# Performance work log

Measured on AMD Instinct MI355X. Metric: run time of the kernel, lower is better.

Reference implementation:

```python
import jax, jax.numpy as jnp
import numpy as np
import math

D_MODEL = 1024
NUM_HEADS = 16
D_KEY = D_MODEL // NUM_HEADS  # 64, used only for the softmax scale
B, S = 4, 2048


def setup_inputs() -> dict:
    key = jax.random.key(0)
    ks = jax.random.split(key, 7)
    scale = 1.0 / math.sqrt(D_MODEL)
    x = jax.random.normal(ks[0], (B, S, D_MODEL), dtype=jnp.float32)
    # torch.nn.Linear params: weight [out, in], bias [out]
    Wq = jax.random.normal(ks[1], (D_MODEL, D_MODEL), dtype=jnp.float32) * scale
    bq = jax.random.normal(ks[2], (D_MODEL,), dtype=jnp.float32) * scale
    Wk = jax.random.normal(ks[3], (D_MODEL, D_MODEL), dtype=jnp.float32) * scale
    bk = jax.random.normal(ks[4], (D_MODEL,), dtype=jnp.float32) * scale
    Wv = jax.random.normal(ks[5], (D_MODEL, D_MODEL), dtype=jnp.float32) * scale
    bv = jax.random.normal(ks[6], (D_MODEL,), dtype=jnp.float32) * scale
    return {"x": x, "Wq": Wq, "bq": bq, "Wk": Wk, "bk": bk, "Wv": Wv, "bv": bv}


def reference(x, Wq, bq, Wk, bk, Wv, bv):
    # Q, K, V projections (torch Linear: x @ W.T + b)
    Q = jnp.einsum('bsd,ed->bse', x, Wq) + bq  # [B,S,D]
    K = jnp.einsum('bsd,ed->bse', x, Wk) + bk
    V = jnp.einsum('bsd,ed->bse', x, Wv) + bv
    inv_sqrt_dk = 1.0 / math.sqrt(D_KEY)
    # full-width attention (no head split, as in the source forward)
    scores = jnp.einsum('bqd,bkd->bqk', Q, K) * inv_sqrt_dk  # [B,S,S]
    weights = jax.nn.softmax(scores, axis=-1)
    return jnp.einsum('bqk,bkd->bqd', weights, V)  # [B,S,D]
```

## Files before the change

kernel.cpp:

```cpp
#include <hip/hip_runtime.h>
#include <stdint.h>

#define S_LEN 2048
#define DMODEL 1024
#define NBATCH 4
#define MROWS (NBATCH * S_LEN)

typedef __bf16 bf16x8 __attribute__((ext_vector_type(8)));
typedef float f32x4 __attribute__((ext_vector_type(4)));

__device__ __forceinline__ unsigned short f2bf(float f) {
  unsigned int x = __builtin_bit_cast(unsigned int, f);
  x += 0x7FFFu + ((x >> 16) & 1u);
  return (unsigned short)(x >> 16);
}

template <int N>
__device__ __forceinline__ void waitvm() {
  static_assert(N <= 8, "vmcnt range");
  if constexpr (N < 0) {}
  else if constexpr (N == 0) asm volatile("s_waitcnt vmcnt(0)" ::: "memory");
  else if constexpr (N == 1) asm volatile("s_waitcnt vmcnt(1)" ::: "memory");
  else if constexpr (N == 2) asm volatile("s_waitcnt vmcnt(2)" ::: "memory");
  else if constexpr (N == 3) asm volatile("s_waitcnt vmcnt(3)" ::: "memory");
  else if constexpr (N == 4) asm volatile("s_waitcnt vmcnt(4)" ::: "memory");
  else if constexpr (N == 5) asm volatile("s_waitcnt vmcnt(5)" ::: "memory");
  else if constexpr (N == 6) asm volatile("s_waitcnt vmcnt(6)" ::: "memory");
  else if constexpr (N == 7) asm volatile("s_waitcnt vmcnt(7)" ::: "memory");
  else asm volatile("s_waitcnt vmcnt(8)" ::: "memory");
}
#define BARRIER() do { __builtin_amdgcn_s_barrier(); asm volatile("" ::: "memory"); } while (0)
#define LGKM0() do { asm volatile("s_waitcnt lgkmcnt(0)" ::: "memory"); \
                     __builtin_amdgcn_sched_barrier(0); } while (0)

__global__ void cvt_kernel(const float* __restrict__ src, ushort4* __restrict__ dst, int n4) {
  int i = blockIdx.x * blockDim.x + threadIdx.x;
  if (i < n4) {
    float4 v = reinterpret_cast<const float4*>(src)[i];
    ushort4 o;
    o.x = f2bf(v.x); o.y = f2bf(v.y); o.z = f2bf(v.z); o.w = f2bf(v.w);
    dst[i] = o;
  }
}

__global__ void prep_kernel(const float* __restrict__ Wq, const float* __restrict__ Wk,
                            const float* __restrict__ Wv, const float* __restrict__ bq,
                            const float* __restrict__ bk, ushort4* __restrict__ Wqkb,
                            ushort4* __restrict__ Wvb, float4* __restrict__ bqk) {
  const int NW = DMODEL * DMODEL / 4;
  int i = blockIdx.x * blockDim.x + threadIdx.x;
  float4 v;
  if (i < NW) v = reinterpret_cast<const float4*>(Wq)[i];
  else if (i < 2 * NW) v = reinterpret_cast<const float4*>(Wk)[i - NW];
  else v = reinterpret_cast<const float4*>(Wv)[i - 2 * NW];
  ushort4 o;
  o.x = f2bf(v.x); o.y = f2bf(v.y); o.z = f2bf(v.z); o.w = f2bf(v.w);
  if (i < 2 * NW) Wqkb[i] = o;
  else Wvb[i - 2 * NW] = o;
  if (i < 512) bqk[i] = (i < 256) ? reinterpret_cast<const float4*>(bq)[i]
                                  : reinterpret_cast<const float4*>(bk)[i - 256];
}

template <int BM_, int EP, int NT>
__global__ __launch_bounds__(512, 2) void gemm8(
    const unsigned short* __restrict__ A, const unsigned short* __restrict__ Bm,
    void* __restrict__ Cp, const float* __restrict__ bias,
    int lda, int ldb, int ldc, float scale,
    long zsA, long zsB, long zsC) {
  constexpr int BN_ = 256;
  constexpr int BK = 64;
  constexpr int RA = BM_ / 128;
  constexpr int HALF_A = (BM_ / 2) * 128;
  constexpr int HALF_B = 128 * 128;
  constexpr int ATILE = BM_ * 128;
  constexpr int BTILE = BN_ * 128;
  constexpr int MREP = BM_ / 32;
  constexpr int MQ = MREP / 2;
  constexpr int VPRO = (BM_ == 256) ? 4 : 3;
  constexpr int W_PA = (BM_ == 256) ? 6 : 4;
  constexpr int W_PB = (BM_ == 256) ? 6 : 5;
  constexpr int W_PC = (BM_ == 256) ? 4 : 3;
  constexpr int VDA  = (BM_ == 256) ? 2 : 1;

  __shared__ alignas(16) char lds[(ATILE + BTILE) * 2];

  const int tid = threadIdx.x;
  const int l = tid & 63;
  const int w = tid >> 6;
  const int wm = w >> 2;
  const int wn = w & 3;

  const int gx = gridDim.x;
  const int nwg = gridDim.x * gridDim.y;
  int n = blockIdx.y * gx + blockIdx.x;
  int n2 = (n & 7) * (nwg >> 3) + (n >> 3);
  const int tileM = (n2 / gx) * BM_;
  const int tileN = (n2 % gx) * BN_;

  const int z = blockIdx.z;
  const unsigned short* Ab = A + (size_t)z * zsA;
  const unsigned short* Bb = Bm + (size_t)z * zsB;

  const int srow = l >> 3;
  const int scol = (((l & 7) ^ srow) * 16);

  auto stageA = [&](int buf, int t, int h) {
#pragma unroll
    for (int r = 0; r < RA; ++r) {
      int row = h * (BM_ / 2) + r * 64 + w * 8 + srow;
      const char* g = (const char*)(Ab + (size_t)(tileM + row) * lda + t * BK) + scol;
      char* d = lds + buf * (ATILE + BTILE) + h * HALF_A + r * 8192 + w * 1024;
      __builtin_amdgcn_global_load_lds(
          (const __attribute__((address_space(1))) void*)g,
          (__attribute__((address_space(3))) void*)d, 16, 0, 0);
    }
  };
  auto stageB = [&](int buf, int t, int h) {
#pragma unroll
    for (int r = 0; r < 2; ++r) {
      int row = h * 128 + r * 64 + w * 8 + srow;
      const char* g = (const char*)(Bb + (size_t)(tileN + row) * ldb + t * BK) + scol;
      char* d = lds + buf * (ATILE + BTILE) + ATILE + h * HALF_B + r * 8192 + w * 1024;
      __builtin_amdgcn_global_load_lds(
          (const __attribute__((address_space(1))) void*)g,
          (__attribute__((address_space(3))) void*)d, 16, 0, 0);
    }
  };

  f32x4 acc[MREP][4];
#pragma unroll
  for (int m = 0; m < MREP; ++m)
#pragma unroll
    for (int nn = 0; nn < 4; ++nn) acc[m][nn] = f32x4{0.f, 0.f, 0.f, 0.f};

  const int frow = l & 15;
  auto rdA = [&](int buf, int mh, int m, int kk) -> bf16x8 {
    int row = mh * (BM_ / 2) + wm * (BM_ / 4) + m * 16 + frow;
    int col = (kk * 64 + ((l >> 4) * 16)) ^ ((row & 7) << 4);
    return *reinterpret_cast<const bf16x8*>(lds + buf * (ATILE + BTILE) + row * 128 + col);
  };
  auto rdB = [&](int buf, int nh, int nn, int kk) -> bf16x8 {
    int row = nh * 128 + wn * 32 + nn * 16 + frow;
    int col = (kk * 64 + ((l >> 4) * 16)) ^ ((row & 7) << 4);
    return *reinterpret_cast<const bf16x8*>(lds + buf * (ATILE + BTILE) + ATILE + row * 128 + col);
  };

  bf16x8 avF[MQ][2];
  bf16x8 bv0[2][2], bv1[2][2];

  auto rdAfull = [&](int buf, int mh) {
#pragma unroll
    for (int m = 0; m < MQ; ++m)
#pragma unroll
      for (int kk = 0; kk < 2; ++kk) avF[m][kk] = rdA(buf, mh, m, kk);
  };
  auto rdBfull = [&](int buf, int nh, bf16x8 (&bv)[2][2]) {
#pragma unroll
    for (int nn = 0; nn < 2; ++nn)
#pragma unroll
      for (int kk = 0; kk < 2; ++kk) bv[nn][kk] = rdB(buf, nh, nn, kk);
  };
  auto mfc = [&](int mh, bf16x8 (&bv)[2][2], int nh) {
    __builtin_amdgcn_s_setprio(1);
#pragma unroll
    for (int kk = 0; kk < 2; ++kk)
#pragma unroll
      for (int m = 0; m < MQ; ++m)
#pragma unroll
        for (int nn = 0; nn < 2; ++nn)
          acc[mh * MQ + m][nh * 2 + nn] = __builtin_amdgcn_mfma_f32_16x16x32_bf16(
              avF[m][kk], bv[nn][kk], acc[mh * MQ + m][nh * 2 + nn], 0, 0, 0);
    __builtin_amdgcn_s_setprio(0);
  };
  auto mfc2 = [&](int mh) {
    __builtin_amdgcn_s_setprio(1);
#pragma unroll
    for (int kk = 0; kk < 2; ++kk)
#pragma unroll
      for (int m = 0; m < MQ; ++m) {
#pragma unroll
        for (int nn = 0; nn < 2; ++nn)
          acc[mh * MQ + m][2 + nn] = __builtin_amdgcn_mfma_f32_16x16x32_bf16(
              avF[m][kk], bv1[nn][kk], acc[mh * MQ + m][2 + nn], 0, 0, 0);
#pragma unroll
        for (int nn = 0; nn < 2; ++nn)
          acc[mh * MQ + m][nn] = __builtin_amdgcn_mfma_f32_16x16x32_bf16(
              avF[m][kk], bv0[nn][kk], acc[mh * MQ + m][nn], 0, 0, 0);
      }
    __builtin_amdgcn_s_setprio(0);
  };

  stageA(0, 0, 0);
  stageB(0, 0, 0);
  stageB(0, 0, 1);
  stageA(0, 0, 1);
  waitvm<VPRO>();
  BARRIER();

#pragma unroll 2
  for (int t = 0; t < NT - 1; ++t) {
    const int buf = t & 1, nb = buf ^ 1;
    rdAfull(buf, 0); rdBfull(buf, 0, bv0);
    stageA(nb, t + 1, 0); stageB(nb, t + 1, 0);
    waitvm<W_PA>(); BARRIER(); LGKM0();
    mfc(0, bv0, 0);
    rdBfull(buf, 1, bv1);
    stageB(nb, t + 1, 1);
    waitvm<W_PB>(); BARRIER(); LGKM0();
    mfc(0, bv1, 1);
    rdAfull(buf, 1);
    stageA(nb, t + 1, 1);
    waitvm<W_PC>(); BARRIER(); LGKM0();
    mfc2(1);
  }
  {
    const int buf = (NT - 1) & 1;
    rdAfull(buf, 0); rdBfull(buf, 0, bv0);
    waitvm<VDA>(); BARRIER(); LGKM0();
    mfc(0, bv0, 0);
    rdBfull(buf, 1, bv1);
    waitvm<0>(); BARRIER(); LGKM0();
    mfc(0, bv1, 1);
    rdAfull(buf, 1);
    LGKM0();
    mfc2(1);
  }

  const int lr = (l >> 4) * 4;
  const int lc = l & 15;
#pragma unroll
  for (int mh = 0; mh < 2; ++mh) {
#pragma unroll
    for (int m = 0; m < MQ; ++m) {
#pragma unroll
      for (int nh = 0; nh < 2; ++nh) {
#pragma unroll
        for (int nn = 0; nn < 2; ++nn) {
          int gr = tileM + mh * (BM_ / 2) + wm * (BM_ / 4) + m * 16 + lr;
          int gc = tileN + nh * 128 + wn * 32 + nn * 16 + lc;
          f32x4 v = acc[mh * MQ + m][nh * 2 + nn];
          if constexpr (EP == 0 || EP == 3) {
            unsigned short* C = (unsigned short*)Cp + (size_t)z * zsC;
#pragma unroll
            for (int j = 0; j < 4; ++j) {
              float bb = (EP == 0) ? bias[gc] : bias[gr + j];
              C[(size_t)(gr + j) * ldc + gc] = f2bf(v[j] + bb);
            }
          } else {
            float* C = (float*)Cp + (size_t)z * zsC;
#pragma unroll
            for (int j = 0; j < 4; ++j)
              C[(size_t)(gr + j) * ldc + gc] = (EP == 1) ? v[j] * scale : v[j];
          }
        }
      }
    }
  }
}

__global__ __launch_bounds__(256) void softmax_kernel(const float* __restrict__ Sb,
                                                      unsigned short* __restrict__ P) {
  const size_t row = blockIdx.x;
  const float* sp = Sb + row * S_LEN;
  const int t = threadIdx.x;
  const int wid = t >> 6, lane = t & 63;
  float4 v0 = reinterpret_cast<const float4*>(sp)[t * 2];
  float4 v1 = reinterpret_cast<const float4*>(sp)[t * 2 + 1];
  float s[8] = {v0.x, v0.y, v0.z, v0.w, v1.x, v1.y, v1.z, v1.w};
  float mx = s[0];
#pragma unroll
  for (int i = 1; i < 8; ++i) mx = fmaxf(mx, s[i]);
#pragma unroll
  for (int o = 32; o > 0; o >>= 1) mx = fmaxf(mx, __shfl_xor(mx, o));
  __shared__ float redm[4];
  __shared__ float reds[4];
  if (lane == 0) redm[wid] = mx;
  __syncthreads();
  mx = fmaxf(fmaxf(redm[0], redm[1]), fmaxf(redm[2], redm[3]));
  float e[8];
  float sum = 0.f;
#pragma unroll
  for (int i = 0; i < 8; ++i) { e[i] = __expf(s[i] - mx); sum += e[i]; }
#pragma unroll
  for (int o = 32; o > 0; o >>= 1) sum += __shfl_xor(sum, o);
  if (lane == 0) reds[wid] = sum;
  __syncthreads();
  sum = reds[0] + reds[1] + reds[2] + reds[3];
  float inv = 1.0f / sum;
  ushort4 o0, o1;
  o0.x = f2bf(e[0] * inv); o0.y = f2bf(e[1] * inv); o0.z = f2bf(e[2] * inv); o0.w = f2bf(e[3] * inv);
  o1.x = f2bf(e[4] * inv); o1.y = f2bf(e[5] * inv); o1.z = f2bf(e[6] * inv); o1.w = f2bf(e[7] * inv);
  ushort4* dp = reinterpret_cast<ushort4*>(P + row * S_LEN);
  dp[t * 2] = o0;
  dp[t * 2 + 1] = o1;
}

extern "C" void kernel_launch(void* const* d_in, const int* in_sizes, int n_in,
                              void* d_out, int out_size, void* d_ws, size_t ws_size,
                              hipStream_t stream) {
  (void)in_sizes; (void)n_in; (void)out_size;
  const float* x = (const float*)d_in[0];
  const float* Wq = (const float*)d_in[1];
  const float* bq = (const float*)d_in[2];
  const float* Wk = (const float*)d_in[3];
  const float* bk = (const float*)d_in[4];
  const float* Wv = (const float*)d_in[5];
  const float* bv = (const float*)d_in[6];
  float* out = (float*)d_out;

  if (ws_size < 141557760ull) return;
  char* ws = (char*)d_ws;
  unsigned short* xb   = (unsigned short*)(ws);
  unsigned short* Wqkb = (unsigned short*)(ws + 16777216);
  unsigned short* Wvb  = (unsigned short*)(ws + 20971520);
  float*          bqk  = (float*)(ws + 23068672);
  unsigned short* QKb  = (unsigned short*)(ws + 24117248);
  float*          Sb   = (float*)(ws + 57671680);
  unsigned short* Vt   = (unsigned short*)(ws + 124780544);
  unsigned short* P    = QKb;

  cvt_kernel<<<dim3(MROWS * DMODEL / 4 / 256), 256, 0, stream>>>(x, (ushort4*)xb, MROWS * DMODEL / 4);
  prep_kernel<<<dim3(3 * DMODEL * DMODEL / 4 / 256), 256, 0, stream>>>(
      Wq, Wk, Wv, bq, bk, (ushort4*)Wqkb, (ushort4*)Wvb, (float4*)bqk);

  gemm8<256, 0, 16><<<dim3(8, 32, 1), 512, 0, stream>>>(
      xb, Wqkb, QKb, bqk, 1024, 1024, 2048, 1.f, 0, 0, 0);

  gemm8<128, 3, 16><<<dim3(8, 8, 4), 512, 0, stream>>>(
      Wvb, xb, Vt, bv, 1024, 1024, 2048, 1.f,
      0, (long)S_LEN * DMODEL, (long)DMODEL * S_LEN);

  gemm8<256, 1, 16><<<dim3(8, 8, 4), 512, 0, stream>>>(
      QKb, QKb + 1024, Sb, nullptr, 2048, 2048, 2048, 0.125f,
      (long)S_LEN * 2048, (long)S_LEN * 2048, (long)S_LEN * S_LEN);

  softmax_kernel<<<dim3(MROWS), 256, 0, stream>>>(Sb, P);

  gemm8<128, 2, 32><<<dim3(4, 16, 4), 512, 0, stream>>>(
      P, Vt, out, nullptr, 2048, 2048, 1024, 1.f,
      (long)S_LEN * S_LEN, (long)DMODEL * S_LEN, (long)S_LEN * DMODEL);
}
```

Measured before the change: 165.9 us.

## Add 16-wave 256x256 GEMM kernel for QK projection and scores; merge prep kernels

Introduces gemm16, a 1024-thread (16 waves) 256x256-tile bf16 MFMA GEMM with a split-phase double-buffered LDS pipeline and XOR-swizzled direct-to-LDS loads. It replaces gemm8 for the fused Q/K projection and for the QK^T score GEMM. The two conversion kernels for x and the weights are also merged into one launch. The aim is more waves per tile to hide latency and one less launch, at the cost of one workgroup per CU, more barriers, and uncoalesced scalar epilogue stores.

```diff
diff --git a/kernel.cpp b/kernel.cpp
--- a/kernel.cpp
+++ b/kernel.cpp
@@ -33,32 +33,208 @@
 #define LGKM0() do { asm volatile("s_waitcnt lgkmcnt(0)" ::: "memory"); \
                      __builtin_amdgcn_sched_barrier(0); } while (0)
 
-__global__ void cvt_kernel(const float* __restrict__ src, ushort4* __restrict__ dst, int n4) {
-  int i = blockIdx.x * blockDim.x + threadIdx.x;
-  if (i < n4) {
-    float4 v = reinterpret_cast<const float4*>(src)[i];
-    ushort4 o;
-    o.x = f2bf(v.x); o.y = f2bf(v.y); o.z = f2bf(v.z); o.w = f2bf(v.w);
-    dst[i] = o;
-  }
-}
-
-__global__ void prep_kernel(const float* __restrict__ Wq, const float* __restrict__ Wk,
-                            const float* __restrict__ Wv, const float* __restrict__ bq,
-                            const float* __restrict__ bk, ushort4* __restrict__ Wqkb,
-                            ushort4* __restrict__ Wvb, float4* __restrict__ bqk) {
+__global__ void prep_all_kernel(const float* __restrict__ x, const float* __restrict__ Wq,
+                                const float* __restrict__ Wk, const float* __restrict__ Wv,
+                                const float* __restrict__ bq, const float* __restrict__ bk,
+                                ushort4* __restrict__ xb, ushort4* __restrict__ Wqkb,
+                                ushort4* __restrict__ Wvb, float4* __restrict__ bqk) {
+  const int NX = MROWS * DMODEL / 4;
   const int NW = DMODEL * DMODEL / 4;
   int i = blockIdx.x * blockDim.x + threadIdx.x;
   float4 v;
-  if (i < NW) v = reinterpret_cast<const float4*>(Wq)[i];
-  else if (i < 2 * NW) v = reinterpret_cast<const float4*>(Wk)[i - NW];
-  else v = reinterpret_cast<const float4*>(Wv)[i - 2 * NW];
-  ushort4 o;
-  o.x = f2bf(v.x); o.y = f2bf(v.y); o.z = f2bf(v.z); o.w = f2bf(v.w);
-  if (i < 2 * NW) Wqkb[i] = o;
-  else Wvb[i - 2 * NW] = o;
-  if (i < 512) bqk[i] = (i < 256) ? reinterpret_cast<const float4*>(bq)[i]
-                                  : reinterpret_cast<const float4*>(bk)[i - 256];
+  if (i < NX) {
+    v = reinterpret_cast<const float4*>(x)[i];
+    ushort4 o; o.x = f2bf(v.x); o.y = f2bf(v.y); o.z = f2bf(v.z); o.w = f2bf(v.w);
+    xb[i] = o;
+  } else {
+    int j = i - NX;
+    if (j < NW) v = reinterpret_cast<const float4*>(Wq)[j];
+    else if (j < 2 * NW) v = reinterpret_cast<const float4*>(Wk)[j - NW];
+    else v = reinterpret_cast<const float4*>(Wv)[j - 2 * NW];
+    ushort4 o; o.x = f2bf(v.x); o.y = f2bf(v.y); o.z = f2bf(v.z); o.w = f2bf(v.w);
+    if (j < 2 * NW) Wqkb[j] = o;
+    else Wvb[j - 2 * NW] = o;
+    if (j < 512) bqk[j] = (j < 256) ? reinterpret_cast<const float4*>(bq)[j]
+                                    : reinterpret_cast<const float4*>(bk)[j - 256];
+  }
+}
+
+template <int EP, int NT>
+__global__ __launch_bounds__(1024, 1) void gemm16(
+    const unsigned short* __restrict__ A, const unsigned short* __restrict__ Bm,
+    void* __restrict__ Cp, const float* __restrict__ bias,
+    int lda, int ldb, int ldc, float scale,
+    long zsA, long zsB, long zsC) {
+  constexpr int BK = 64;
+  constexpr int ATILE = 256 * 128;
+  constexpr int TILE2 = ATILE * 2;
+  constexpr int HALF = 128 * 128;
+
+  __shared__ alignas(16) char lds[TILE2 * 2];
+
+  const int tid = threadIdx.x;
+  const int l = tid & 63;
+  const int w = tid >> 6;
+  const int wm = w >> 2;
+  const int wn = w & 3;
+
+  const int gx = gridDim.x;
+  const int nwg = gridDim.x * gridDim.y;
+  int n = blockIdx.y * gx + blockIdx.x;
+  int n2 = (n & 7) * (nwg >> 3) + (n >> 3);
+  const int tileM = (n2 / gx) * 256;
+  const int tileN = (n2 % gx) * 256;
+
+  const int z = blockIdx.z;
+  const unsigned short* Ab = A + (size_t)z * zsA;
+  const unsigned short* Bb = Bm + (size_t)z * zsB;
+
+  const int srow = l >> 3;
+  const int scol = (((l & 7) ^ srow) * 16);
+
+  auto stageA = [&](int buf, int t, int h) {
+    int row = h * 128 + w * 8 + srow;
+    const char* g = (const char*)(Ab + (size_t)(tileM + row) * lda + t * BK) + scol;
+    char* d = lds + buf * TILE2 + h * HALF + w * 1024;
+    __builtin_amdgcn_global_load_lds(
+        (const __attribute__((address_space(1))) void*)g,
+        (__attribute__((address_space(3))) void*)d, 16, 0, 0);
+  };
+  auto stageB = [&](int buf, int t, int h) {
+    int row = h * 128 + w * 8 + srow;
+    const char* g = (const char*)(Bb + (size_t)(tileN + row) * ldb + t * BK) + scol;
+    char* d = lds + buf * TILE2 + ATILE + h * HALF + w * 1024;
+    __builtin_amdgcn_global_load_lds(
+        (const __attribute__((address_space(1))) void*)g,
+        (__attribute__((address_space(3))) void*)d, 16, 0, 0);
+  };
+
+  f32x4 acc[4][4];
+#pragma unroll
+  for (int m = 0; m < 4; ++m)
+#pragma unroll
+    for (int nn = 0; nn < 4; ++nn) acc[m][nn] = f32x4{0.f, 0.f, 0.f, 0.f};
+
+  const int frow = l & 15;
+  auto rdA = [&](int buf, int mh, int m, int kk) -> bf16x8 {
+    int row = mh * 128 + wm * 32 + m * 16 + frow;
+    int col = (kk * 64 + ((l >> 4) * 16)) ^ ((row & 7) << 4);
+    return *reinterpret_cast<const bf16x8*>(lds + buf * TILE2 + row * 128 + col);
+  };
+  auto rdB = [&](int buf, int nh, int nn, int kk) -> bf16x8 {
+    int row = nh * 128 + wn * 32 + nn * 16 + frow;
+    int col = (kk * 64 + ((l >> 4) * 16)) ^ ((row & 7) << 4);
+    return *reinterpret_cast<const bf16x8*>(lds + buf * TILE2 + ATILE + row * 128 + col);
+  };
+
+  bf16x8 avF[2][2];
+  bf16x8 bv0[2][2], bv1[2][2];
+
+  auto rdAfull = [&](int buf, int mh) {
+#pragma unroll
+    for (int m = 0; m < 2; ++m)
+#pragma unroll
+      for (int kk = 0; kk < 2; ++kk) avF[m][kk] = rdA(buf, mh, m, kk);
+  };
+  auto rdBfull = [&](int buf, int nh, bf16x8 (&bv)[2][2]) {
+#pragma unroll
+    for (int nn = 0; nn < 2; ++nn)
+#pragma unroll
+      for (int kk = 0; kk < 2; ++kk) bv[nn][kk] = rdB(buf, nh, nn, kk);
+  };
+  auto mfc = [&](int mh, bf16x8 (&bv)[2][2], int nh) {
+    __builtin_amdgcn_s_setprio(1);
+#pragma unroll
+    for (int kk = 0; kk < 2; ++kk)
+#pragma unroll
+      for (int m = 0; m < 2; ++m)
+#pragma unroll
+        for (int nn = 0; nn < 2; ++nn)
+          acc[mh * 2 + m][nh * 2 + nn] = __builtin_amdgcn_mfma_f32_16x16x32_bf16(
+              avF[m][kk], bv[nn][kk], acc[mh * 2 + m][nh * 2 + nn], 0, 0, 0);
+    __builtin_amdgcn_s_setprio(0);
+  };
+  auto mfc2 = [&](int mh) {
+    __builtin_amdgcn_s_setprio(1);
+#pragma unroll
+    for (int kk = 0; kk < 2; ++kk)
+#pragma unroll
+      for (int m = 0; m < 2; ++m) {
+#pragma unroll
+        for (int nn = 0; nn < 2; ++nn)
+          acc[mh * 2 + m][2 + nn] = __builtin_amdgcn_mfma_f32_16x16x32_bf16(
+              avF[m][kk], bv1[nn][kk], acc[mh * 2 + m][2 + nn], 0, 0, 0);
+#pragma unroll
+        for (int nn = 0; nn < 2; ++nn)
+          acc[mh * 2 + m][nn] = __builtin_amdgcn_mfma_f32_16x16x32_bf16(
+              avF[m][kk], bv0[nn][kk], acc[mh * 2 + m][nn], 0, 0, 0);
+      }
+    __builtin_amdgcn_s_setprio(0);
+  };
+
+  stageA(0, 0, 0);
+  stageB(0, 0, 0);
+  stageB(0, 0, 1);
+  stageA(0, 0, 1);
+  waitvm<2>();
+  BARRIER();
+
+#pragma unroll 2
+  for (int t = 0; t < NT - 1; ++t) {
+    const int buf = t & 1, nb = buf ^ 1;
+    rdAfull(buf, 0); rdBfull(buf, 0, bv0);
+    stageA(nb, t + 1, 0); stageB(nb, t + 1, 0);
+    waitvm<3>(); BARRIER(); LGKM0();
+    mfc(0, bv0, 0);
+    rdBfull(buf, 1, bv1);
+    stageB(nb, t + 1, 1);
+    waitvm<3>(); BARRIER(); LGKM0();
+    mfc(0, bv1, 1);
+    rdAfull(buf, 1);
+    stageA(nb, t + 1, 1);
+    waitvm<2>(); BARRIER(); LGKM0();
+    mfc2(1);
+  }
+  {
+    const int buf = (NT - 1) & 1;
+    rdAfull(buf, 0); rdBfull(buf, 0, bv0);
+    waitvm<1>(); BARRIER(); LGKM0();
+    mfc(0, bv0, 0);
+    rdBfull(buf, 1, bv1);
+    waitvm<0>(); BARRIER(); LGKM0();
+    mfc(0, bv1, 1);
+    rdAfull(buf, 1);
+    LGKM0();
+    mfc2(1);
+  }
+
+  const int lr = (l >> 4) * 4;
+  const int lc = l & 15;
+#pragma unroll
+  for (int mh = 0; mh < 2; ++mh) {
+#pragma unroll
+    for (int m = 0; m < 2; ++m) {
+#pragma unroll
+      for (int nh = 0; nh < 2; ++nh) {
+#pragma unroll
+        for (int nn = 0; nn < 2; ++nn) {
+          int gr = tileM + mh * 128 + wm * 32 + m * 16 + lr;
+          int gc = tileN + nh * 128 + wn * 32 + nn * 16 + lc;
+          f32x4 v = acc[mh * 2 + m][nh * 2 + nn];
+          if constexpr (EP == 0) {
+            unsigned short* C = (unsigned short*)Cp + (size_t)z * zsC;
+            float bb = bias[gc];
+#pragma unroll
+            for (int j = 0; j < 4; ++j) C[(size_t)(gr + j) * ldc + gc] = f2bf(v[j] + bb);
+          } else {
+            float* C = (float*)Cp + (size_t)z * zsC;
+#pragma unroll
+            for (int j = 0; j < 4; ++j) C[(size_t)(gr + j) * ldc + gc] = v[j] * scale;
+          }
+        }
+      }
+    }
+  }
 }
 
 template <int BM_, int EP, int NT>
@@ -319,18 +495,18 @@
   unsigned short* Vt   = (unsigned short*)(ws + 124780544);
   unsigned short* P    = QKb;
 
-  cvt_kernel<<<dim3(MROWS * DMODEL / 4 / 256), 256, 0, stream>>>(x, (ushort4*)xb, MROWS * DMODEL / 4);
-  prep_kernel<<<dim3(3 * DMODEL * DMODEL / 4 / 256), 256, 0, stream>>>(
-      Wq, Wk, Wv, bq, bk, (ushort4*)Wqkb, (ushort4*)Wvb, (float4*)bqk);
-
-  gemm8<256, 0, 16><<<dim3(8, 32, 1), 512, 0, stream>>>(
+  const int NX = MROWS * DMODEL / 4, NW = DMODEL * DMODEL / 4;
+  prep_all_kernel<<<dim3((NX + 3 * NW) / 256), 256, 0, stream>>>(
+      x, Wq, Wk, Wv, bq, bk, (ushort4*)xb, (ushort4*)Wqkb, (ushort4*)Wvb, (float4*)bqk);
+
+  gemm16<0, 16><<<dim3(8, 32, 1), 1024, 0, stream>>>(
       xb, Wqkb, QKb, bqk, 1024, 1024, 2048, 1.f, 0, 0, 0);
 
   gemm8<128, 3, 16><<<dim3(8, 8, 4), 512, 0, stream>>>(
       Wvb, xb, Vt, bv, 1024, 1024, 2048, 1.f,
       0, (long)S_LEN * DMODEL, (long)DMODEL * S_LEN);
 
-  gemm8<256, 1, 16><<<dim3(8, 8, 4), 512, 0, stream>>>(
+  gemm16<1, 16><<<dim3(8, 8, 4), 1024, 0, stream>>>(
       QKb, QKb + 1024, Sb, nullptr, 2048, 2048, 2048, 0.125f,
       (long)S_LEN * 2048, (long)S_LEN * 2048, (long)S_LEN * S_LEN);
 
```

Measured after the change: 171.3 us. 3.3% more time.

## Merge conversion kernels and simplify GEMM pipeline to one barrier per K-step

Applied to the files above, without the earlier changes.

Combines the x conversion and weight/bias prep kernels into a single launch, removing one kernel launch. In the bf16 GEMM main loop, the three staged vmcnt waits and barriers per K-iteration are replaced by a single full drain (lgkmcnt(0), vmcnt(0)) and one barrier at the end of each iteration. The sched_barrier fences are dropped, so the compiler is free to reorder LDS reads and MFMAs. This cuts barrier count, but a full vmcnt(0) drain per iteration reduces how much global-to-LDS prefetch overlaps with compute, and it loses the hand-tuned interleaving.

```diff
diff --git a/kernel.cpp b/kernel.cpp
--- a/kernel.cpp
+++ b/kernel.cpp
@@ -30,35 +30,32 @@
   else asm volatile("s_waitcnt vmcnt(8)" ::: "memory");
 }
 #define BARRIER() do { __builtin_amdgcn_s_barrier(); asm volatile("" ::: "memory"); } while (0)
-#define LGKM0() do { asm volatile("s_waitcnt lgkmcnt(0)" ::: "memory"); \
-                     __builtin_amdgcn_sched_barrier(0); } while (0)
-
-__global__ void cvt_kernel(const float* __restrict__ src, ushort4* __restrict__ dst, int n4) {
-  int i = blockIdx.x * blockDim.x + threadIdx.x;
-  if (i < n4) {
-    float4 v = reinterpret_cast<const float4*>(src)[i];
-    ushort4 o;
-    o.x = f2bf(v.x); o.y = f2bf(v.y); o.z = f2bf(v.z); o.w = f2bf(v.w);
-    dst[i] = o;
-  }
-}
-
-__global__ void prep_kernel(const float* __restrict__ Wq, const float* __restrict__ Wk,
-                            const float* __restrict__ Wv, const float* __restrict__ bq,
-                            const float* __restrict__ bk, ushort4* __restrict__ Wqkb,
-                            ushort4* __restrict__ Wvb, float4* __restrict__ bqk) {
+#define LGKM0() asm volatile("s_waitcnt lgkmcnt(0)" ::: "memory")
+
+__global__ void prep_all_kernel(const float* __restrict__ x, const float* __restrict__ Wq,
+                                const float* __restrict__ Wk, const float* __restrict__ Wv,
+                                const float* __restrict__ bq, const float* __restrict__ bk,
+                                ushort4* __restrict__ xb, ushort4* __restrict__ Wqkb,
+                                ushort4* __restrict__ Wvb, float4* __restrict__ bqk) {
+  const int NX = MROWS * DMODEL / 4;
   const int NW = DMODEL * DMODEL / 4;
   int i = blockIdx.x * blockDim.x + threadIdx.x;
   float4 v;
-  if (i < NW) v = reinterpret_cast<const float4*>(Wq)[i];
-  else if (i < 2 * NW) v = reinterpret_cast<const float4*>(Wk)[i - NW];
-  else v = reinterpret_cast<const float4*>(Wv)[i - 2 * NW];
-  ushort4 o;
-  o.x = f2bf(v.x); o.y = f2bf(v.y); o.z = f2bf(v.z); o.w = f2bf(v.w);
-  if (i < 2 * NW) Wqkb[i] = o;
-  else Wvb[i - 2 * NW] = o;
-  if (i < 512) bqk[i] = (i < 256) ? reinterpret_cast<const float4*>(bq)[i]
-                                  : reinterpret_cast<const float4*>(bk)[i - 256];
+  if (i < NX) {
+    v = reinterpret_cast<const float4*>(x)[i];
+    ushort4 o; o.x = f2bf(v.x); o.y = f2bf(v.y); o.z = f2bf(v.z); o.w = f2bf(v.w);
+    xb[i] = o;
+  } else {
+    int j = i - NX;
+    if (j < NW) v = reinterpret_cast<const float4*>(Wq)[j];
+    else if (j < 2 * NW) v = reinterpret_cast<const float4*>(Wk)[j - NW];
+    else v = reinterpret_cast<const float4*>(Wv)[j - 2 * NW];
+    ushort4 o; o.x = f2bf(v.x); o.y = f2bf(v.y); o.z = f2bf(v.z); o.w = f2bf(v.w);
+    if (j < 2 * NW) Wqkb[j] = o;
+    else Wvb[j - 2 * NW] = o;
+    if (j < 512) bqk[j] = (j < 256) ? reinterpret_cast<const float4*>(bq)[j]
+                                    : reinterpret_cast<const float4*>(bk)[j - 256];
+  }
 }
 
 template <int BM_, int EP, int NT>
@@ -76,11 +73,6 @@
   constexpr int BTILE = BN_ * 128;
   constexpr int MREP = BM_ / 32;
   constexpr int MQ = MREP / 2;
-  constexpr int VPRO = (BM_ == 256) ? 4 : 3;
-  constexpr int W_PA = (BM_ == 256) ? 6 : 4;
-  constexpr int W_PB = (BM_ == 256) ? 6 : 5;
-  constexpr int W_PC = (BM_ == 256) ? 4 : 3;
-  constexpr int VDA  = (BM_ == 256) ? 2 : 1;
 
   __shared__ alignas(16) char lds[(ATILE + BTILE) * 2];
 
@@ -194,7 +186,7 @@
   stageB(0, 0, 0);
   stageB(0, 0, 1);
   stageA(0, 0, 1);
-  waitvm<VPRO>();
+  waitvm<0>();
   BARRIER();
 
 #pragma unroll 2
@@ -202,27 +194,24 @@
     const int buf = t & 1, nb = buf ^ 1;
     rdAfull(buf, 0); rdBfull(buf, 0, bv0);
     stageA(nb, t + 1, 0); stageB(nb, t + 1, 0);
-    waitvm<W_PA>(); BARRIER(); LGKM0();
     mfc(0, bv0, 0);
     rdBfull(buf, 1, bv1);
     stageB(nb, t + 1, 1);
-    waitvm<W_PB>(); BARRIER(); LGKM0();
     mfc(0, bv1, 1);
     rdAfull(buf, 1);
     stageA(nb, t + 1, 1);
-    waitvm<W_PC>(); BARRIER(); LGKM0();
     mfc2(1);
+    LGKM0();
+    waitvm<0>();
+    BARRIER();
   }
   {
     const int buf = (NT - 1) & 1;
     rdAfull(buf, 0); rdBfull(buf, 0, bv0);
-    waitvm<VDA>(); BARRIER(); LGKM0();
     mfc(0, bv0, 0);
     rdBfull(buf, 1, bv1);
-    waitvm<0>(); BARRIER(); LGKM0();
     mfc(0, bv1, 1);
     rdAfull(buf, 1);
-    LGKM0();
     mfc2(1);
   }
 
@@ -319,9 +308,9 @@
   unsigned short* Vt   = (unsigned short*)(ws + 124780544);
   unsigned short* P    = QKb;
 
-  cvt_kernel<<<dim3(MROWS * DMODEL / 4 / 256), 256, 0, stream>>>(x, (ushort4*)xb, MROWS * DMODEL / 4);
-  prep_kernel<<<dim3(3 * DMODEL * DMODEL / 4 / 256), 256, 0, stream>>>(
-      Wq, Wk, Wv, bq, bk, (ushort4*)Wqkb, (ushort4*)Wvb, (float4*)bqk);
+  const int NX = MROWS * DMODEL / 4, NW = DMODEL * DMODEL / 4;
+  prep_all_kernel<<<dim3((NX + 3 * NW) / 256), 256, 0, stream>>>(
+      x, Wq, Wk, Wv, bq, bk, (ushort4*)xb, (ushort4*)Wqkb, (ushort4*)Wvb, (float4*)bqk);
 
   gemm8<256, 0, 16><<<dim3(8, 32, 1), 512, 0, stream>>>(
       xb, Wqkb, QKb, bqk, 1024, 1024, 2048, 1.f, 0, 0, 0);
```

Result: no change. 169.2 us (+2.0%).
